# Optimization experiments

Hardware: AMD Instinct MI355X
Metric: run time of the kernel (lower is better)

The kernel has to match this reference:

```python
import jax, jax.numpy as jnp
import numpy as np

D_G, D_2D, D_3D = 512, 768, 1024
D_F, RANK, ATTN_H = 256, 16, 512
B = 8192


def _xavier(key, shape):
    fan_out, fan_in = shape
    lim = float(np.sqrt(6.0 / (fan_in + fan_out)))
    return jax.random.uniform(key, shape, jnp.float32, -lim, lim)


def setup_inputs() -> dict:
    key = jax.random.key(0)
    ks = jax.random.split(key, 12)
    inp = {
        "h_g": jax.random.normal(ks[0], (B, D_G), jnp.float32),
        "h_2d": jax.random.normal(ks[1], (B, D_2D), jnp.float32),
        "h_3d": jax.random.normal(ks[2], (B, D_3D), jnp.float32),
        # modality projections (torch Linear: y = x @ W.T + b)
        "Wg": _xavier(ks[3], (D_F, D_G)),   "bg": jnp.zeros((D_F,), jnp.float32),
        "W2": _xavier(ks[4], (D_F, D_2D)),  "b2": jnp.zeros((D_F,), jnp.float32),
        "W3": _xavier(ks[5], (D_F, D_3D)),  "b3": jnp.zeros((D_F,), jnp.float32),
        # LayerNorm affine params
        "ln_g_w": jnp.ones((D_F,), jnp.float32),  "ln_g_b": jnp.zeros((D_F,), jnp.float32),
        "ln_2_w": jnp.ones((D_F,), jnp.float32),  "ln_2_b": jnp.zeros((D_F,), jnp.float32),
        "ln_3_w": jnp.ones((D_F,), jnp.float32),  "ln_3_b": jnp.zeros((D_F,), jnp.float32),
        # rank expansions (no bias)
        "U": _xavier(ks[6], (RANK * D_F, D_F)),
        "V": _xavier(ks[7], (RANK * D_F, D_F)),
        "S": _xavier(ks[8], (RANK * D_F, D_F)),
        # attention MLP
        "Wa1": _xavier(ks[9], (ATTN_H, D_G + D_2D + D_3D)), "ba1": jnp.zeros((ATTN_H,), jnp.float32),
        "Wa2": _xavier(ks[10], (RANK, ATTN_H)),             "ba2": jnp.zeros((RANK,), jnp.float32),
    }
    return inp


def _layernorm(x, w, b, eps=1e-5):
    mu = jnp.mean(x, axis=-1, keepdims=True)
    var = jnp.var(x, axis=-1, keepdims=True)
    return (x - mu) * jax.lax.rsqrt(var + eps) * w + b


def reference(h_g, h_2d, h_3d, Wg, bg, W2, b2, W3, b3,
              ln_g_w, ln_g_b, ln_2_w, ln_2_b, ln_3_w, ln_3_b,
              U, V, S, Wa1, ba1, Wa2, ba2):
    # proj + LN + ReLU (dropout=0 / eval mode)
    g = jax.nn.relu(_layernorm(h_g @ Wg.T + bg, ln_g_w, ln_g_b))
    d2 = jax.nn.relu(_layernorm(h_2d @ W2.T + b2, ln_2_w, ln_2_b))
    d3 = jax.nn.relu(_layernorm(h_3d @ W3.T + b3, ln_3_w, ln_3_b))
    b = g.shape[0]
    # rank expansion: (B, R, d_f)
    g_r = (g @ U.T).reshape(b, RANK, D_F)
    d2_r = (d2 @ V.T).reshape(b, RANK, D_F)
    d3_r = (d3 @ S.T).reshape(b, RANK, D_F)
    z_r = g_r * d2_r * d3_r  # elementwise tri-linear product
    # rank attention from raw modality concat
    h_cat = jnp.concatenate([h_g, h_2d, h_3d], axis=-1)
    beta = jax.nn.softmax(jax.nn.relu(h_cat @ Wa1.T + ba1) @ Wa2.T + ba2, axis=-1)  # (B, R)
    z = jnp.einsum('brd,br->bd', z_r, beta)  # (B, d_f)
    return z
```

## Files before the change

### kernel.cpp

```cpp
#include <hip/hip_runtime.h>
#include <stdint.h>

#define B_ROWS 8192
#define DG 512
#define D2 768
#define D3 1024
#define DCAT 2304
#define DF 256
#define RANK 16
#define AH 512

#define OFF_WG 0
#define OFF_W2 131072
#define OFF_W3 327680
#define OFF_U  589824
#define OFF_V  1638400
#define OFF_S  2686976
#define OFF_WA1 3735552

#define WS_WBUF  0u
#define WS_HCAT  9830400u
#define WS_GBUF  9830400u
#define WS_PROJ  47579136u
#define WS_A1P   72744960u
#define WS_BETA  89522176u
#define WS_ZPART 47579136u
#define WS_REQUIRED 94240768u

typedef __attribute__((ext_vector_type(8))) short short8;
typedef __attribute__((ext_vector_type(4))) float f32x4;

__device__ inline unsigned short f2bf(float f) {
  union { float f; unsigned int u; } v; v.f = f;
  unsigned int u = v.u + 0x7fffu + ((v.u >> 16) & 1u);
  return (unsigned short)(u >> 16);
}
__device__ inline float bf2f(unsigned short h) {
  union { float f; unsigned int u; } v; v.u = ((unsigned int)h) << 16;
  return v.f;
}

typedef const unsigned int __attribute__((address_space(1)))* as1_u32p;
typedef unsigned int __attribute__((address_space(3)))* as3_u32p;

__device__ inline void g2l16(const unsigned short* g, unsigned short* l) {
  __builtin_amdgcn_global_load_lds((as1_u32p)g, (as3_u32p)l, 16, 0, 0);
}


__global__ __launch_bounds__(256) void cvt_all_k(const float* __restrict__ hg,
                                                 const float* __restrict__ h2,
                                                 const float* __restrict__ h3,
                                                 const float* __restrict__ Wg,
                                                 const float* __restrict__ W2,
                                                 const float* __restrict__ W3,
                                                 const float* __restrict__ U,
                                                 const float* __restrict__ V,
                                                 const float* __restrict__ S,
                                                 const float* __restrict__ Wa1,
                                                 unsigned short* __restrict__ hcat,
                                                 unsigned short* __restrict__ wbuf) {
  const int bid = blockIdx.x;
  if (bid < 18432) {
    const int idx = bid * 256 + threadIdx.x;
    const int e = idx * 4;
    const int row = e / DCAT;
    const int col = e - row * DCAT;
    const float* src;
    if (col < DG) src = hg + (size_t)row * DG + col;
    else if (col < DG + D2) src = h2 + (size_t)row * D2 + (col - DG);
    else src = h3 + (size_t)row * D3 + (col - DG - D2);
    float4 v = *(const float4*)src;
    ushort4 o;
    o.x = f2bf(v.x); o.y = f2bf(v.y); o.z = f2bf(v.z); o.w = f2bf(v.w);
    *(ushort4*)(hcat + e) = o;
  } else {
    const int idx = (bid - 18432) * 256 + threadIdx.x;
    const int e = idx * 4;
    const float* src;
    if (e < OFF_W2)       src = Wg  + e;
    else if (e < OFF_W3)  src = W2  + (e - OFF_W2);
    else if (e < OFF_U)   src = W3  + (e - OFF_W3);
    else if (e < OFF_V)   src = U   + (e - OFF_U);
    else if (e < OFF_S)   src = V   + (e - OFF_V);
    else if (e < OFF_WA1) src = S   + (e - OFF_S);
    else                  src = Wa1 + (e - OFF_WA1);
    float4 v = *(const float4*)src;
    ushort4 o;
    o.x = f2bf(v.x); o.y = f2bf(v.y); o.z = f2bf(v.z); o.w = f2bf(v.w);
    *(ushort4*)(wbuf + e) = o;
  }
}


__device__ __forceinline__ void gemm_mainloop(const unsigned short* Ag, int lda,
                                              const unsigned short* Bg, int ldb,
                                              int K,
                                              unsigned short* lA, unsigned short* lB,
                                              f32x4 acc[4][4]) {
  const int tid = threadIdx.x;
  const int lane = tid & 63;
  const int wr = tid >> 7;
  const int wc = (tid >> 6) & 1;
#pragma unroll
  for (int i = 0; i < 4; ++i)
#pragma unroll
    for (int j = 0; j < 4; ++j)
      acc[i][j] = (f32x4){0.f, 0.f, 0.f, 0.f};

  const int row_s = tid >> 3;
  const int kc_s = (((tid & 7) ^ ((tid >> 3) & 7)) << 3);
  const int mbase = wr * 64 + (lane & 15);
  const int nbase = wc * 64 + (lane & 15);
  const int kq = lane >> 4;
  const int h = lane & 7;

  const int nsteps = K >> 6;
  for (int ks = 0; ks < nsteps; ++ks) {
    const int k0 = ks << 6;
    __syncthreads();
#pragma unroll
    for (int p = 0; p < 4; ++p) {
      const int row = p * 32 + row_s;
      const int lofs = (p * 256 + tid) * 8;
      g2l16(Ag + (size_t)row * lda + k0 + kc_s, lA + lofs);
      g2l16(Bg + (size_t)row * ldb + k0 + kc_s, lB + lofs);
    }
    __syncthreads();
#pragma unroll
    for (int kk = 0; kk < 2; ++kk) {
      const int kch = (kk << 2) + kq;
      const int ko = ((kch ^ h) << 3);
      short8 af[4], bfr[4];
#pragma unroll
      for (int t = 0; t < 4; ++t) {
        af[t]  = *(const short8*)(lA + (mbase + t * 16) * 64 + ko);
        bfr[t] = *(const short8*)(lB + (nbase + t * 16) * 64 + ko);
      }
#pragma unroll
      for (int ti = 0; ti < 4; ++ti)
#pragma unroll
        for (int tj = 0; tj < 4; ++tj)
          acc[ti][tj] = __builtin_amdgcn_mfma_f32_16x16x32_bf16(af[ti], bfr[tj], acc[ti][tj], 0, 0, 0);
    }
  }
}


__device__ __forceinline__ void gemm_mainloop_bk128(const unsigned short* Ag, int lda,
                                                    const unsigned short* Bg, int ldb,
                                                    int K,
                                                    unsigned short* lA, unsigned short* lB,
                                                    f32x4 acc[4][4]) {
  const int tid = threadIdx.x;
  const int lane = tid & 63;
  const int wr = tid >> 7;
  const int wc = (tid >> 6) & 1;
#pragma unroll
  for (int i = 0; i < 4; ++i)
#pragma unroll
    for (int j = 0; j < 4; ++j)
      acc[i][j] = (f32x4){0.f, 0.f, 0.f, 0.f};

  const int row_s = tid >> 4;
  const int kc_s = (((tid & 15) ^ ((tid >> 4) & 15)) << 3);
  const int mbase = wr * 64 + (lane & 15);
  const int nbase = wc * 64 + (lane & 15);
  const int kq = lane >> 4;
  const int h = lane & 15;

  const int nsteps = K >> 7;
  for (int ks = 0; ks < nsteps; ++ks) {
    const int k0 = ks << 7;
    __syncthreads();
#pragma unroll
    for (int p = 0; p < 8; ++p) {
      const int row = p * 16 + row_s;
      const int lofs = (p * 256 + tid) * 8;
      g2l16(Ag + (size_t)row * lda + k0 + kc_s, lA + lofs);
      g2l16(Bg + (size_t)row * ldb + k0 + kc_s, lB + lofs);
    }
    __syncthreads();
#pragma unroll
    for (int kk = 0; kk < 4; ++kk) {
      const int kch = (kk << 2) + kq;
      const int ko = ((kch ^ h) << 3);
      short8 af[4], bfr[4];
#pragma unroll
      for (int t = 0; t < 4; ++t) {
        af[t]  = *(const short8*)(lA + (mbase + t * 16) * 128 + ko);
        bfr[t] = *(const short8*)(lB + (nbase + t * 16) * 128 + ko);
      }
#pragma unroll
      for (int ti = 0; ti < 4; ++ti)
#pragma unroll
        for (int tj = 0; tj < 4; ++tj)
          acc[ti][tj] = __builtin_amdgcn_mfma_f32_16x16x32_bf16(af[ti], bfr[tj], acc[ti][tj], 0, 0, 0);
    }
  }
}


__global__ __launch_bounds__(256) void fatgemm_k(const unsigned short* __restrict__ hcat,
                                                 const unsigned short* __restrict__ wbuf,
                                                 float* __restrict__ proj,
                                                 unsigned short* __restrict__ a1part) {
  __shared__ __align__(16) unsigned short lA[128 * 64];
  __shared__ __align__(16) unsigned short lB[128 * 64];
  const int bid = blockIdx.x;
  f32x4 acc[4][4];
  const int lane = threadIdx.x & 63;
  const int wr = threadIdx.x >> 7, wc = (threadIdx.x >> 6) & 1;

  if (bid < 384) {
    const int z = bid >> 7;
    const int local = bid & 127;
    const int m0 = (local >> 1) << 7;
    const int n0 = (local & 1) << 7;
    const int Kz   = (z == 0) ? DG : (z == 1 ? D2 : D3);
    const int aoff = (z == 0) ? 0  : (z == 1 ? DG : DG + D2);
    const int woff = (z == 0) ? OFF_WG : (z == 1 ? OFF_W2 : OFF_W3);
    gemm_mainloop(hcat + (size_t)m0 * DCAT + aoff, DCAT,
                  wbuf + woff + (size_t)n0 * Kz, Kz, Kz, lA, lB, acc);
    float* out = proj + (size_t)z * B_ROWS * DF;
    const int r0 = m0 + wr * 64 + ((lane >> 4) << 2);
    const int c0 = n0 + wc * 64 + (lane & 15);
#pragma unroll
    for (int ti = 0; ti < 4; ++ti)
#pragma unroll
      for (int tj = 0; tj < 4; ++tj)
#pragma unroll
        for (int i = 0; i < 4; ++i)
          out[(size_t)(r0 + ti * 16 + i) * DF + (c0 + tj * 16)] = acc[ti][tj][i];
  } else {
    const int t = bid - 384;
    const int half = t >> 8;
    const int local = t & 255;
    const int m0 = (local >> 2) << 7;
    const int n0 = (local & 3) << 7;
    const int koff = half * 1152;
    gemm_mainloop(hcat + (size_t)m0 * DCAT + koff, DCAT,
                  wbuf + OFF_WA1 + (size_t)n0 * DCAT + koff, DCAT, 1152, lA, lB, acc);
    unsigned short* out = a1part + (size_t)half * (B_ROWS * AH);
    const int r0 = m0 + wr * 64 + ((lane >> 4) << 2);
    const int c0 = n0 + wc * 64 + (lane & 15);
#pragma unroll
    for (int ti = 0; ti < 4; ++ti)
#pragma unroll
      for (int tj = 0; tj < 4; ++tj)
#pragma unroll
        for (int i = 0; i < 4; ++i)
          out[(size_t)(r0 + ti * 16 + i) * AH + (c0 + tj * 16)] = f2bf(acc[ti][tj][i]);
  }
}


__global__ __launch_bounds__(256) void rank_fused_k(const unsigned short* __restrict__ gbuf,
                                                    const unsigned short* __restrict__ wbuf,
                                                    const float* __restrict__ beta,
                                                    float* __restrict__ zpart) {
  __shared__ __align__(16) unsigned short lA[128 * 128];
  __shared__ __align__(16) unsigned short lB[128 * 128];
  __shared__ float lbeta[4 * 128];
  const int m0 = blockIdx.x * 128;
  const int d0 = blockIdx.y * 128;
  const int rg = blockIdx.z * 4;

  for (int i = threadIdx.x; i < 512; i += 256) {
    const int rr = i >> 7, row = i & 127;
    lbeta[i] = beta[(size_t)(m0 + row) * RANK + rg + rr];
  }

  const int lane = threadIdx.x & 63;
  const int wr = threadIdx.x >> 7, wc = (threadIdx.x >> 6) & 1;
  const int lr0 = wr * 64 + ((lane >> 4) << 2);

  f32x4 zacc[4][4];
#pragma unroll
  for (int ti = 0; ti < 4; ++ti)
#pragma unroll
    for (int tj = 0; tj < 4; ++tj)
      zacc[ti][tj] = (f32x4){0.f, 0.f, 0.f, 0.f};

  for (int rr = 0; rr < 4; ++rr) {
    const int n0 = (rg + rr) * 256 + d0;
    f32x4 prod[4][4];
    f32x4 acc[4][4];
#pragma unroll
    for (int zi = 0; zi < 3; ++zi) {
      gemm_mainloop_bk128(gbuf + (size_t)zi * B_ROWS * DF + (size_t)m0 * DF, DF,
                          wbuf + OFF_U + (size_t)zi * 1048576 + (size_t)n0 * DF, DF, DF,
                          lA, lB, acc);
      if (zi == 0) {
#pragma unroll
        for (int ti = 0; ti < 4; ++ti)
#pragma unroll
          for (int tj = 0; tj < 4; ++tj)
            prod[ti][tj] = acc[ti][tj];
      } else {
#pragma unroll
        for (int ti = 0; ti < 4; ++ti)
#pragma unroll
          for (int tj = 0; tj < 4; ++tj)
            prod[ti][tj] *= acc[ti][tj];
      }
    }
#pragma unroll
    for (int ti = 0; ti < 4; ++ti) {
      const float4 b4 = *(const float4*)(lbeta + rr * 128 + lr0 + ti * 16);
      const float bv[4] = {b4.x, b4.y, b4.z, b4.w};
#pragma unroll
      for (int tj = 0; tj < 4; ++tj)
#pragma unroll
        for (int i = 0; i < 4; ++i)
          zacc[ti][tj][i] += prod[ti][tj][i] * bv[i];
    }
  }

  float* zp = zpart + (size_t)blockIdx.z * (B_ROWS * DF);
  const int c0 = d0 + wc * 64 + (lane & 15);
#pragma unroll
  for (int ti = 0; ti < 4; ++ti)
#pragma unroll
    for (int tj = 0; tj < 4; ++tj)
#pragma unroll
      for (int i = 0; i < 4; ++i)
        zp[(size_t)(m0 + lr0 + ti * 16 + i) * DF + (c0 + tj * 16)] = zacc[ti][tj][i];
}


__global__ __launch_bounds__(256) void zsum_k(const float* __restrict__ zpart,
                                              float* __restrict__ z) {
  const int idx = blockIdx.x * 256 + threadIdx.x;
  const size_t e = (size_t)idx * 4;
  const size_t stride = (size_t)B_ROWS * DF;
  float4 a = *(const float4*)(zpart + e);
  float4 b = *(const float4*)(zpart + stride + e);
  float4 c = *(const float4*)(zpart + 2 * stride + e);
  float4 d = *(const float4*)(zpart + 3 * stride + e);
  float4 o;
  o.x = (a.x + b.x) + (c.x + d.x);
  o.y = (a.y + b.y) + (c.y + d.y);
  o.z = (a.z + b.z) + (c.z + d.z);
  o.w = (a.w + b.w) + (c.w + d.w);
  *(float4*)(z + e) = o;
}


__global__ __launch_bounds__(256) void ln_relu_k(const float* __restrict__ proj,
                                                 const float* __restrict__ bg, const float* __restrict__ b2, const float* __restrict__ b3,
                                                 const float* __restrict__ wg, const float* __restrict__ wbg,
                                                 const float* __restrict__ w2, const float* __restrict__ wb2,
                                                 const float* __restrict__ w3, const float* __restrict__ wb3,
                                                 unsigned short* __restrict__ gout) {
  const int gid = blockIdx.x * 4 + (threadIdx.x >> 6);
  const int lane = threadIdx.x & 63;
  const int z = gid >> 13;
  const int row = gid & (B_ROWS - 1);
  const float* bias = z == 0 ? bg : (z == 1 ? b2 : b3);
  const float* lw = z == 0 ? wg : (z == 1 ? w2 : w3);
  const float* lb = z == 0 ? wbg : (z == 1 ? wb2 : wb3);
  const float* x = proj + (size_t)z * B_ROWS * DF + (size_t)row * DF + lane * 4;
  float4 v = *(const float4*)x;
  float4 bb = *(const float4*)(bias + lane * 4);
  v.x += bb.x; v.y += bb.y; v.z += bb.z; v.w += bb.w;
  float s = v.x + v.y + v.z + v.w;
  float q = v.x * v.x + v.y * v.y + v.z * v.z + v.w * v.w;
#pragma unroll
  for (int m = 1; m < 64; m <<= 1) { s += __shfl_xor(s, m, 64); q += __shfl_xor(q, m, 64); }
  const float mean = s * (1.f / DF);
  const float var = q * (1.f / DF) - mean * mean;
  const float rs = rsqrtf(var + 1e-5f);
  float4 w4 = *(const float4*)(lw + lane * 4);
  float4 b4 = *(const float4*)(lb + lane * 4);
  ushort4 o;
  o.x = f2bf(fmaxf((v.x - mean) * rs * w4.x + b4.x, 0.f));
  o.y = f2bf(fmaxf((v.y - mean) * rs * w4.y + b4.y, 0.f));
  o.z = f2bf(fmaxf((v.z - mean) * rs * w4.z + b4.z, 0.f));
  o.w = f2bf(fmaxf((v.w - mean) * rs * w4.w + b4.w, 0.f));
  *(ushort4*)(gout + (size_t)z * B_ROWS * DF + (size_t)row * DF + lane * 4) = o;
}


__global__ __launch_bounds__(256) void attn_beta_k(const unsigned short* __restrict__ a1part,
                                                   const float* __restrict__ ba1,
                                                   const float* __restrict__ Wa2,
                                                   const float* __restrict__ ba2,
                                                   float* __restrict__ beta) {
  __shared__ float lw[RANK * AH];
  for (int i = threadIdx.x; i < RANK * AH / 4; i += 256)
    *(float4*)(lw + i * 4) = *(const float4*)(Wa2 + i * 4);
  __syncthreads();
  const int row = blockIdx.x * 4 + (threadIdx.x >> 6);
  const int lane = threadIdx.x & 63;
  const unsigned short* h0 = a1part + (size_t)row * AH + lane * 8;
  const unsigned short* h1 = h0 + (size_t)B_ROWS * AH;
  const uint4 p0 = *(const uint4*)h0;
  const uint4 p1 = *(const uint4*)h1;
  const unsigned int u0[4] = {p0.x, p0.y, p0.z, p0.w};
  const unsigned int u1[4] = {p1.x, p1.y, p1.z, p1.w};
  float4 ca = *(const float4*)(ba1 + lane * 8);
  float4 cb = *(const float4*)(ba1 + lane * 8 + 4);
  const float bias[8] = {ca.x, ca.y, ca.z, ca.w, cb.x, cb.y, cb.z, cb.w};
  float av[8];
#pragma unroll
  for (int j = 0; j < 4; ++j) {
    const float s0 = bf2f((unsigned short)(u0[j] & 0xffffu)) + bf2f((unsigned short)(u1[j] & 0xffffu));
    const float s1 = bf2f((unsigned short)(u0[j] >> 16)) + bf2f((unsigned short)(u1[j] >> 16));
    av[2 * j]     = fmaxf(s0 + bias[2 * j], 0.f);
    av[2 * j + 1] = fmaxf(s1 + bias[2 * j + 1], 0.f);
  }
  float lg[RANK];
#pragma unroll
  for (int r = 0; r < RANK; ++r) {
    const float* wrow = lw + r * AH + lane * 8;
    float4 wa = *(const float4*)wrow;
    float4 wb = *(const float4*)(wrow + 4);
    float p = av[0] * wa.x + av[1] * wa.y + av[2] * wa.z + av[3] * wa.w
            + av[4] * wb.x + av[5] * wb.y + av[6] * wb.z + av[7] * wb.w;
#pragma unroll
    for (int m = 1; m < 64; m <<= 1) p += __shfl_xor(p, m, 64);
    lg[r] = p + ba2[r];
  }
  float mx = lg[0];
#pragma unroll
  for (int r = 1; r < RANK; ++r) mx = fmaxf(mx, lg[r]);
  float den = 0.f;
#pragma unroll
  for (int r = 0; r < RANK; ++r) { lg[r] = __expf(lg[r] - mx); den += lg[r]; }
  const float inv = 1.f / den;
  if (lane < RANK) {
    float mine = 0.f;
#pragma unroll
    for (int r = 0; r < RANK; ++r) mine = (lane == r) ? lg[r] : mine;
    beta[(size_t)row * RANK + lane] = mine * inv;
  }
}


extern "C" void kernel_launch(void* const* d_in, const int* in_sizes, int n_in,
                              void* d_out, int out_size, void* d_ws, size_t ws_size,
                              hipStream_t stream) {
  if (ws_size < (size_t)WS_REQUIRED) return;

  const float* h_g   = (const float*)d_in[0];
  const float* h_2d  = (const float*)d_in[1];
  const float* h_3d  = (const float*)d_in[2];
  const float* Wg    = (const float*)d_in[3];
  const float* bg    = (const float*)d_in[4];
  const float* W2    = (const float*)d_in[5];
  const float* b2    = (const float*)d_in[6];
  const float* W3    = (const float*)d_in[7];
  const float* b3    = (const float*)d_in[8];
  const float* ln_g_w = (const float*)d_in[9];
  const float* ln_g_b = (const float*)d_in[10];
  const float* ln_2_w = (const float*)d_in[11];
  const float* ln_2_b = (const float*)d_in[12];
  const float* ln_3_w = (const float*)d_in[13];
  const float* ln_3_b = (const float*)d_in[14];
  const float* U     = (const float*)d_in[15];
  const float* V     = (const float*)d_in[16];
  const float* S     = (const float*)d_in[17];
  const float* Wa1   = (const float*)d_in[18];
  const float* ba1   = (const float*)d_in[19];
  const float* Wa2   = (const float*)d_in[20];
  const float* ba2   = (const float*)d_in[21];

  char* ws = (char*)d_ws;
  unsigned short* wbuf   = (unsigned short*)(ws + WS_WBUF);
  unsigned short* hcat   = (unsigned short*)(ws + WS_HCAT);
  unsigned short* gbuf   = (unsigned short*)(ws + WS_GBUF);
  float*          proj   = (float*)(ws + WS_PROJ);
  unsigned short* a1part = (unsigned short*)(ws + WS_A1P);
  float*          beta   = (float*)(ws + WS_BETA);
  float*          zpart  = (float*)(ws + WS_ZPART);
  float* z = (float*)d_out;

  cvt_all_k<<<dim3(23232), dim3(256), 0, stream>>>(h_g, h_2d, h_3d,
                                                   Wg, W2, W3, U, V, S, Wa1, hcat, wbuf);
  fatgemm_k<<<dim3(896), dim3(256), 0, stream>>>(hcat, wbuf, proj, a1part);
  ln_relu_k<<<dim3(6144), dim3(256), 0, stream>>>(proj, bg, b2, b3, ln_g_w, ln_g_b,
                                                  ln_2_w, ln_2_b, ln_3_w, ln_3_b, gbuf);
  attn_beta_k<<<dim3(2048), dim3(256), 0, stream>>>(a1part, ba1, Wa2, ba2, beta);
  rank_fused_k<<<dim3(64, 2, 4), dim3(256), 0, stream>>>(gbuf, wbuf, beta, zpart);
  zsum_k<<<dim3(2048), dim3(256), 0, stream>>>(zpart, z);
}
```

Measured before the change: 324.6 us.

## Double-buffer rank GEMM LDS stages and merge LN and attention-beta kernels

The rank-fused kernel now runs a single flattened loop over all 48 K-steps (4 ranks × 3 modalities × 4 K-chunks of 64). It double-buffers the LDS tiles so the next global-to-LDS load is issued before the current tile's MFMAs, and it needs one barrier per step instead of two. The LayerNorm/ReLU kernel and the attention softmax kernel are merged into one launch, with blocks split by index. LDS use drops from 64KB to 64KB total across two buffers of half-K, and the merged kernel carries the larger shared-memory footprint for all blocks.

```diff
diff --git a/kernel.cpp b/kernel.cpp
--- a/kernel.cpp
+++ b/kernel.cpp
@@ -147,60 +147,6 @@
 }
 
 
-__device__ __forceinline__ void gemm_mainloop_bk128(const unsigned short* Ag, int lda,
-                                                    const unsigned short* Bg, int ldb,
-                                                    int K,
-                                                    unsigned short* lA, unsigned short* lB,
-                                                    f32x4 acc[4][4]) {
-  const int tid = threadIdx.x;
-  const int lane = tid & 63;
-  const int wr = tid >> 7;
-  const int wc = (tid >> 6) & 1;
-#pragma unroll
-  for (int i = 0; i < 4; ++i)
-#pragma unroll
-    for (int j = 0; j < 4; ++j)
-      acc[i][j] = (f32x4){0.f, 0.f, 0.f, 0.f};
-
-  const int row_s = tid >> 4;
-  const int kc_s = (((tid & 15) ^ ((tid >> 4) & 15)) << 3);
-  const int mbase = wr * 64 + (lane & 15);
-  const int nbase = wc * 64 + (lane & 15);
-  const int kq = lane >> 4;
-  const int h = lane & 15;
-
-  const int nsteps = K >> 7;
-  for (int ks = 0; ks < nsteps; ++ks) {
-    const int k0 = ks << 7;
-    __syncthreads();
-#pragma unroll
-    for (int p = 0; p < 8; ++p) {
-      const int row = p * 16 + row_s;
-      const int lofs = (p * 256 + tid) * 8;
-      g2l16(Ag + (size_t)row * lda + k0 + kc_s, lA + lofs);
-      g2l16(Bg + (size_t)row * ldb + k0 + kc_s, lB + lofs);
-    }
-    __syncthreads();
-#pragma unroll
-    for (int kk = 0; kk < 4; ++kk) {
-      const int kch = (kk << 2) + kq;
-      const int ko = ((kch ^ h) << 3);
-      short8 af[4], bfr[4];
-#pragma unroll
-      for (int t = 0; t < 4; ++t) {
-        af[t]  = *(const short8*)(lA + (mbase + t * 16) * 128 + ko);
-        bfr[t] = *(const short8*)(lB + (nbase + t * 16) * 128 + ko);
-      }
-#pragma unroll
-      for (int ti = 0; ti < 4; ++ti)
-#pragma unroll
-        for (int tj = 0; tj < 4; ++tj)
-          acc[ti][tj] = __builtin_amdgcn_mfma_f32_16x16x32_bf16(af[ti], bfr[tj], acc[ti][tj], 0, 0, 0);
-    }
-  }
-}
-
-
 __global__ __launch_bounds__(256) void fatgemm_k(const unsigned short* __restrict__ hcat,
                                                  const unsigned short* __restrict__ wbuf,
                                                  float* __restrict__ proj,
@@ -259,61 +205,112 @@
                                                     const unsigned short* __restrict__ wbuf,
                                                     const float* __restrict__ beta,
                                                     float* __restrict__ zpart) {
-  __shared__ __align__(16) unsigned short lA[128 * 128];
-  __shared__ __align__(16) unsigned short lB[128 * 128];
+  __shared__ __align__(16) unsigned short lA[2 * 128 * 64];
+  __shared__ __align__(16) unsigned short lB[2 * 128 * 64];
   __shared__ float lbeta[4 * 128];
   const int m0 = blockIdx.x * 128;
   const int d0 = blockIdx.y * 128;
   const int rg = blockIdx.z * 4;
-
-  for (int i = threadIdx.x; i < 512; i += 256) {
+  const int tid = threadIdx.x;
+
+  for (int i = tid; i < 512; i += 256) {
     const int rr = i >> 7, row = i & 127;
     lbeta[i] = beta[(size_t)(m0 + row) * RANK + rg + rr];
   }
 
-  const int lane = threadIdx.x & 63;
-  const int wr = threadIdx.x >> 7, wc = (threadIdx.x >> 6) & 1;
+  const int lane = tid & 63;
+  const int wr = tid >> 7, wc = (tid >> 6) & 1;
+  const int row_s = tid >> 3;
+  const int kc_s = (((tid & 7) ^ ((tid >> 3) & 7)) << 3);
+  const int mbase = wr * 64 + (lane & 15);
+  const int nbase = wc * 64 + (lane & 15);
+  const int kq = lane >> 4;
+  const int h = lane & 7;
   const int lr0 = wr * 64 + ((lane >> 4) << 2);
 
-  f32x4 zacc[4][4];
+  auto stage = [&](int s, int buf) {
+    const int rr = s / 12;
+    const int t  = s - rr * 12;
+    const int zi = t >> 2;
+    const int ks = t & 3;
+    const unsigned short* Ag = gbuf + (size_t)zi * (B_ROWS * DF) + (size_t)m0 * DF + (ks << 6);
+    const unsigned short* Bg = wbuf + OFF_U + (size_t)zi * 1048576
+                             + (size_t)((rg + rr) * 256 + d0) * DF + (ks << 6);
+    unsigned short* dA = lA + buf * 8192;
+    unsigned short* dB = lB + buf * 8192;
+#pragma unroll
+    for (int p = 0; p < 4; ++p) {
+      const int row = p * 32 + row_s;
+      const int lofs = (p * 256 + tid) * 8;
+      g2l16(Ag + (size_t)row * DF + kc_s, dA + lofs);
+      g2l16(Bg + (size_t)row * DF + kc_s, dB + lofs);
+    }
+  };
+
+  f32x4 zacc[4][4], prod[4][4], acc[4][4];
 #pragma unroll
   for (int ti = 0; ti < 4; ++ti)
 #pragma unroll
-    for (int tj = 0; tj < 4; ++tj)
+    for (int tj = 0; tj < 4; ++tj) {
       zacc[ti][tj] = (f32x4){0.f, 0.f, 0.f, 0.f};
-
-  for (int rr = 0; rr < 4; ++rr) {
-    const int n0 = (rg + rr) * 256 + d0;
-    f32x4 prod[4][4];
-    f32x4 acc[4][4];
-#pragma unroll
-    for (int zi = 0; zi < 3; ++zi) {
-      gemm_mainloop_bk128(gbuf + (size_t)zi * B_ROWS * DF + (size_t)m0 * DF, DF,
-                          wbuf + OFF_U + (size_t)zi * 1048576 + (size_t)n0 * DF, DF, DF,
-                          lA, lB, acc);
+      acc[ti][tj]  = (f32x4){0.f, 0.f, 0.f, 0.f};
+    }
+
+  stage(0, 0);
+  for (int s = 0; s < 48; ++s) {
+    const int cur = s & 1;
+    __syncthreads();
+    if (s + 1 < 48) stage(s + 1, cur ^ 1);
+    const unsigned short* sA = lA + cur * 8192;
+    const unsigned short* sB = lB + cur * 8192;
+#pragma unroll
+    for (int kk = 0; kk < 2; ++kk) {
+      const int kch = (kk << 2) + kq;
+      const int ko = ((kch ^ h) << 3);
+      short8 af[4], bfr[4];
+#pragma unroll
+      for (int t = 0; t < 4; ++t) {
+        af[t]  = *(const short8*)(sA + (mbase + t * 16) * 64 + ko);
+        bfr[t] = *(const short8*)(sB + (nbase + t * 16) * 64 + ko);
+      }
+#pragma unroll
+      for (int ti = 0; ti < 4; ++ti)
+#pragma unroll
+        for (int tj = 0; tj < 4; ++tj)
+          acc[ti][tj] = __builtin_amdgcn_mfma_f32_16x16x32_bf16(af[ti], bfr[tj], acc[ti][tj], 0, 0, 0);
+    }
+    if ((s & 3) == 3) {
+      const int rr = s / 12;
+      const int zi = (s - rr * 12) >> 2;
       if (zi == 0) {
 #pragma unroll
         for (int ti = 0; ti < 4; ++ti)
 #pragma unroll
           for (int tj = 0; tj < 4; ++tj)
             prod[ti][tj] = acc[ti][tj];
-      } else {
+      } else if (zi == 1) {
 #pragma unroll
         for (int ti = 0; ti < 4; ++ti)
 #pragma unroll
           for (int tj = 0; tj < 4; ++tj)
             prod[ti][tj] *= acc[ti][tj];
+      } else {
+#pragma unroll
+        for (int ti = 0; ti < 4; ++ti) {
+          const float4 b4 = *(const float4*)(lbeta + rr * 128 + lr0 + ti * 16);
+          const float bv[4] = {b4.x, b4.y, b4.z, b4.w};
+#pragma unroll
+          for (int tj = 0; tj < 4; ++tj)
+#pragma unroll
+            for (int i = 0; i < 4; ++i)
+              zacc[ti][tj][i] += prod[ti][tj][i] * acc[ti][tj][i] * bv[i];
+        }
       }
-    }
-#pragma unroll
-    for (int ti = 0; ti < 4; ++ti) {
-      const float4 b4 = *(const float4*)(lbeta + rr * 128 + lr0 + ti * 16);
-      const float bv[4] = {b4.x, b4.y, b4.z, b4.w};
-#pragma unroll
-      for (int tj = 0; tj < 4; ++tj)
-#pragma unroll
-        for (int i = 0; i < 4; ++i)
-          zacc[ti][tj][i] += prod[ti][tj][i] * bv[i];
+#pragma unroll
+      for (int ti = 0; ti < 4; ++ti)
+#pragma unroll
+        for (int tj = 0; tj < 4; ++tj)
+          acc[ti][tj] = (f32x4){0.f, 0.f, 0.f, 0.f};
     }
   }
 
@@ -347,93 +344,94 @@
 }
 
 
-__global__ __launch_bounds__(256) void ln_relu_k(const float* __restrict__ proj,
-                                                 const float* __restrict__ bg, const float* __restrict__ b2, const float* __restrict__ b3,
-                                                 const float* __restrict__ wg, const float* __restrict__ wbg,
-                                                 const float* __restrict__ w2, const float* __restrict__ wb2,
-                                                 const float* __restrict__ w3, const float* __restrict__ wb3,
-                                                 unsigned short* __restrict__ gout) {
-  const int gid = blockIdx.x * 4 + (threadIdx.x >> 6);
-  const int lane = threadIdx.x & 63;
-  const int z = gid >> 13;
-  const int row = gid & (B_ROWS - 1);
-  const float* bias = z == 0 ? bg : (z == 1 ? b2 : b3);
-  const float* lw = z == 0 ? wg : (z == 1 ? w2 : w3);
-  const float* lb = z == 0 ? wbg : (z == 1 ? wb2 : wb3);
-  const float* x = proj + (size_t)z * B_ROWS * DF + (size_t)row * DF + lane * 4;
-  float4 v = *(const float4*)x;
-  float4 bb = *(const float4*)(bias + lane * 4);
-  v.x += bb.x; v.y += bb.y; v.z += bb.z; v.w += bb.w;
-  float s = v.x + v.y + v.z + v.w;
-  float q = v.x * v.x + v.y * v.y + v.z * v.z + v.w * v.w;
-#pragma unroll
-  for (int m = 1; m < 64; m <<= 1) { s += __shfl_xor(s, m, 64); q += __shfl_xor(q, m, 64); }
-  const float mean = s * (1.f / DF);
-  const float var = q * (1.f / DF) - mean * mean;
-  const float rs = rsqrtf(var + 1e-5f);
-  float4 w4 = *(const float4*)(lw + lane * 4);
-  float4 b4 = *(const float4*)(lb + lane * 4);
-  ushort4 o;
-  o.x = f2bf(fmaxf((v.x - mean) * rs * w4.x + b4.x, 0.f));
-  o.y = f2bf(fmaxf((v.y - mean) * rs * w4.y + b4.y, 0.f));
-  o.z = f2bf(fmaxf((v.z - mean) * rs * w4.z + b4.z, 0.f));
-  o.w = f2bf(fmaxf((v.w - mean) * rs * w4.w + b4.w, 0.f));
-  *(ushort4*)(gout + (size_t)z * B_ROWS * DF + (size_t)row * DF + lane * 4) = o;
-}
-
-
-__global__ __launch_bounds__(256) void attn_beta_k(const unsigned short* __restrict__ a1part,
-                                                   const float* __restrict__ ba1,
-                                                   const float* __restrict__ Wa2,
-                                                   const float* __restrict__ ba2,
-                                                   float* __restrict__ beta) {
-  __shared__ float lw[RANK * AH];
-  for (int i = threadIdx.x; i < RANK * AH / 4; i += 256)
-    *(float4*)(lw + i * 4) = *(const float4*)(Wa2 + i * 4);
-  __syncthreads();
-  const int row = blockIdx.x * 4 + (threadIdx.x >> 6);
-  const int lane = threadIdx.x & 63;
-  const unsigned short* h0 = a1part + (size_t)row * AH + lane * 8;
-  const unsigned short* h1 = h0 + (size_t)B_ROWS * AH;
-  const uint4 p0 = *(const uint4*)h0;
-  const uint4 p1 = *(const uint4*)h1;
-  const unsigned int u0[4] = {p0.x, p0.y, p0.z, p0.w};
-  const unsigned int u1[4] = {p1.x, p1.y, p1.z, p1.w};
-  float4 ca = *(const float4*)(ba1 + lane * 8);
-  float4 cb = *(const float4*)(ba1 + lane * 8 + 4);
-  const float bias[8] = {ca.x, ca.y, ca.z, ca.w, cb.x, cb.y, cb.z, cb.w};
-  float av[8];
-#pragma unroll
-  for (int j = 0; j < 4; ++j) {
-    const float s0 = bf2f((unsigned short)(u0[j] & 0xffffu)) + bf2f((unsigned short)(u1[j] & 0xffffu));
-    const float s1 = bf2f((unsigned short)(u0[j] >> 16)) + bf2f((unsigned short)(u1[j] >> 16));
-    av[2 * j]     = fmaxf(s0 + bias[2 * j], 0.f);
-    av[2 * j + 1] = fmaxf(s1 + bias[2 * j + 1], 0.f);
-  }
-  float lg[RANK];
-#pragma unroll
-  for (int r = 0; r < RANK; ++r) {
-    const float* wrow = lw + r * AH + lane * 8;
-    float4 wa = *(const float4*)wrow;
-    float4 wb = *(const float4*)(wrow + 4);
-    float p = av[0] * wa.x + av[1] * wa.y + av[2] * wa.z + av[3] * wa.w
-            + av[4] * wb.x + av[5] * wb.y + av[6] * wb.z + av[7] * wb.w;
-#pragma unroll
-    for (int m = 1; m < 64; m <<= 1) p += __shfl_xor(p, m, 64);
-    lg[r] = p + ba2[r];
-  }
-  float mx = lg[0];
-#pragma unroll
-  for (int r = 1; r < RANK; ++r) mx = fmaxf(mx, lg[r]);
-  float den = 0.f;
-#pragma unroll
-  for (int r = 0; r < RANK; ++r) { lg[r] = __expf(lg[r] - mx); den += lg[r]; }
-  const float inv = 1.f / den;
-  if (lane < RANK) {
-    float mine = 0.f;
-#pragma unroll
-    for (int r = 0; r < RANK; ++r) mine = (lane == r) ? lg[r] : mine;
-    beta[(size_t)row * RANK + lane] = mine * inv;
+__global__ __launch_bounds__(256) void post_k(const float* __restrict__ proj,
+                                              const float* __restrict__ bg, const float* __restrict__ b2, const float* __restrict__ b3,
+                                              const float* __restrict__ wg, const float* __restrict__ wbg,
+                                              const float* __restrict__ w2, const float* __restrict__ wb2,
+                                              const float* __restrict__ w3, const float* __restrict__ wb3,
+                                              unsigned short* __restrict__ gout,
+                                              const unsigned short* __restrict__ a1part,
+                                              const float* __restrict__ ba1,
+                                              const float* __restrict__ Wa2,
+                                              const float* __restrict__ ba2,
+                                              float* __restrict__ beta) {
+  const int bid = blockIdx.x;
+  if (bid < 6144) {
+    const int gid = bid * 4 + (threadIdx.x >> 6);
+    const int lane = threadIdx.x & 63;
+    const int z = gid >> 13;
+    const int row = gid & (B_ROWS - 1);
+    const float* bias = z == 0 ? bg : (z == 1 ? b2 : b3);
+    const float* lw = z == 0 ? wg : (z == 1 ? w2 : w3);
+    const float* lb = z == 0 ? wbg : (z == 1 ? wb2 : wb3);
+    const float* x = proj + (size_t)z * B_ROWS * DF + (size_t)row * DF + lane * 4;
+    float4 v = *(const float4*)x;
+    float4 bb = *(const float4*)(bias + lane * 4);
+    v.x += bb.x; v.y += bb.y; v.z += bb.z; v.w += bb.w;
+    float s = v.x + v.y + v.z + v.w;
+    float q = v.x * v.x + v.y * v.y + v.z * v.z + v.w * v.w;
+#pragma unroll
+    for (int m = 1; m < 64; m <<= 1) { s += __shfl_xor(s, m, 64); q += __shfl_xor(q, m, 64); }
+    const float mean = s * (1.f / DF);
+    const float var = q * (1.f / DF) - mean * mean;
+    const float rs = rsqrtf(var + 1e-5f);
+    float4 w4 = *(const float4*)(lw + lane * 4);
+    float4 b4 = *(const float4*)(lb + lane * 4);
+    ushort4 o;
+    o.x = f2bf(fmaxf((v.x - mean) * rs * w4.x + b4.x, 0.f));
+    o.y = f2bf(fmaxf((v.y - mean) * rs * w4.y + b4.y, 0.f));
+    o.z = f2bf(fmaxf((v.z - mean) * rs * w4.z + b4.z, 0.f));
+    o.w = f2bf(fmaxf((v.w - mean) * rs * w4.w + b4.w, 0.f));
+    *(ushort4*)(gout + (size_t)z * B_ROWS * DF + (size_t)row * DF + lane * 4) = o;
+  } else {
+    __shared__ float lw[RANK * AH];
+    for (int i = threadIdx.x; i < RANK * AH / 4; i += 256)
+      *(float4*)(lw + i * 4) = *(const float4*)(Wa2 + i * 4);
+    __syncthreads();
+    const int row = (bid - 6144) * 4 + (threadIdx.x >> 6);
+    const int lane = threadIdx.x & 63;
+    const unsigned short* h0 = a1part + (size_t)row * AH + lane * 8;
+    const unsigned short* h1 = h0 + (size_t)B_ROWS * AH;
+    const uint4 p0 = *(const uint4*)h0;
+    const uint4 p1 = *(const uint4*)h1;
+    const unsigned int u0[4] = {p0.x, p0.y, p0.z, p0.w};
+    const unsigned int u1[4] = {p1.x, p1.y, p1.z, p1.w};
+    float4 ca = *(const float4*)(ba1 + lane * 8);
+    float4 cb = *(const float4*)(ba1 + lane * 8 + 4);
+    const float bias[8] = {ca.x, ca.y, ca.z, ca.w, cb.x, cb.y, cb.z, cb.w};
+    float av[8];
+#pragma unroll
+    for (int j = 0; j < 4; ++j) {
+      const float s0 = bf2f((unsigned short)(u0[j] & 0xffffu)) + bf2f((unsigned short)(u1[j] & 0xffffu));
+      const float s1 = bf2f((unsigned short)(u0[j] >> 16)) + bf2f((unsigned short)(u1[j] >> 16));
+      av[2 * j]     = fmaxf(s0 + bias[2 * j], 0.f);
+      av[2 * j + 1] = fmaxf(s1 + bias[2 * j + 1], 0.f);
+    }
+    float lg[RANK];
+#pragma unroll
+    for (int r = 0; r < RANK; ++r) {
+      const float* wrow = lw + r * AH + lane * 8;
+      float4 wa = *(const float4*)wrow;
+      float4 wb = *(const float4*)(wrow + 4);
+      float p = av[0] * wa.x + av[1] * wa.y + av[2] * wa.z + av[3] * wa.w
+              + av[4] * wb.x + av[5] * wb.y + av[6] * wb.z + av[7] * wb.w;
+#pragma unroll
+      for (int m = 1; m < 64; m <<= 1) p += __shfl_xor(p, m, 64);
+      lg[r] = p + ba2[r];
+    }
+    float mx = lg[0];
+#pragma unroll
+    for (int r = 1; r < RANK; ++r) mx = fmaxf(mx, lg[r]);
+    float den = 0.f;
+#pragma unroll
+    for (int r = 0; r < RANK; ++r) { lg[r] = __expf(lg[r] - mx); den += lg[r]; }
+    const float inv = 1.f / den;
+    if (lane < RANK) {
+      float mine = 0.f;
+#pragma unroll
+      for (int r = 0; r < RANK; ++r) mine = (lane == r) ? lg[r] : mine;
+      beta[(size_t)row * RANK + lane] = mine * inv;
+    }
   }
 }
 
@@ -479,9 +477,9 @@
   cvt_all_k<<<dim3(23232), dim3(256), 0, stream>>>(h_g, h_2d, h_3d,
                                                    Wg, W2, W3, U, V, S, Wa1, hcat, wbuf);
   fatgemm_k<<<dim3(896), dim3(256), 0, stream>>>(hcat, wbuf, proj, a1part);
-  ln_relu_k<<<dim3(6144), dim3(256), 0, stream>>>(proj, bg, b2, b3, ln_g_w, ln_g_b,
-                                                  ln_2_w, ln_2_b, ln_3_w, ln_3_b, gbuf);
-  attn_beta_k<<<dim3(2048), dim3(256), 0, stream>>>(a1part, ba1, Wa2, ba2, beta);
+  post_k<<<dim3(8192), dim3(256), 0, stream>>>(proj, bg, b2, b3, ln_g_w, ln_g_b,
+                                               ln_2_w, ln_2_b, ln_3_w, ln_3_b, gbuf,
+                                               a1part, ba1, Wa2, ba2, beta);
   rank_fused_k<<<dim3(64, 2, 4), dim3(256), 0, stream>>>(gbuf, wbuf, beta, zpart);
   zsum_k<<<dim3(2048), dim3(256), 0, stream>>>(zpart, z);
 }
```

Result: slower. 348.5 us (+7.4%).

## Store modality inputs as separate bf16 buffers and merge LN and attention kernels

Applied to the files above, without the earlier changes.

The conversion kernel now writes each modality input into its own contiguous bf16 buffer instead of one interleaved concat matrix, which removes the per-element row/column divide and branch. The projection GEMM reads these directly with a natural stride. The attention GEMM runs two back-to-back accumulating mainloops over the g and 2d parts for one half and the 3d part for the other. The LayerNorm/ReLU and attention-softmax kernels are merged into one launch to save a kernel launch and let the two overlap. The risk is that the merged kernel's attention blocks reserve LDS that the LN blocks do not need, which can lower occupancy, and that the split mainloops add extra sync points.

```diff
diff --git a/kernel.cpp b/kernel.cpp
--- a/kernel.cpp
+++ b/kernel.cpp
@@ -19,7 +19,9 @@
 #define OFF_WA1 3735552
 
 #define WS_WBUF  0u
-#define WS_HCAT  9830400u
+#define WS_HG    9830400u
+#define WS_H2    18219008u
+#define WS_H3    30801920u
 #define WS_GBUF  9830400u
 #define WS_PROJ  47579136u
 #define WS_A1P   72744960u
@@ -48,36 +50,32 @@
 }
 
 
-__global__ __launch_bounds__(256) void cvt_all_k(const float* __restrict__ hg,
-                                                 const float* __restrict__ h2,
-                                                 const float* __restrict__ h3,
-                                                 const float* __restrict__ Wg,
-                                                 const float* __restrict__ W2,
-                                                 const float* __restrict__ W3,
-                                                 const float* __restrict__ U,
-                                                 const float* __restrict__ V,
-                                                 const float* __restrict__ S,
-                                                 const float* __restrict__ Wa1,
-                                                 unsigned short* __restrict__ hcat,
-                                                 unsigned short* __restrict__ wbuf) {
+__global__ __launch_bounds__(256) void cvt_split_k(const float* __restrict__ hg,
+                                                   const float* __restrict__ h2,
+                                                   const float* __restrict__ h3,
+                                                   const float* __restrict__ Wg,
+                                                   const float* __restrict__ W2,
+                                                   const float* __restrict__ W3,
+                                                   const float* __restrict__ U,
+                                                   const float* __restrict__ V,
+                                                   const float* __restrict__ S,
+                                                   const float* __restrict__ Wa1,
+                                                   unsigned short* __restrict__ hgb,
+                                                   unsigned short* __restrict__ h2b,
+                                                   unsigned short* __restrict__ h3b,
+                                                   unsigned short* __restrict__ wbuf) {
   const int bid = blockIdx.x;
+  const float* src;
+  unsigned short* dst;
+  int e;
   if (bid < 18432) {
-    const int idx = bid * 256 + threadIdx.x;
-    const int e = idx * 4;
-    const int row = e / DCAT;
-    const int col = e - row * DCAT;
-    const float* src;
-    if (col < DG) src = hg + (size_t)row * DG + col;
-    else if (col < DG + D2) src = h2 + (size_t)row * D2 + (col - DG);
-    else src = h3 + (size_t)row * D3 + (col - DG - D2);
-    float4 v = *(const float4*)src;
-    ushort4 o;
-    o.x = f2bf(v.x); o.y = f2bf(v.y); o.z = f2bf(v.z); o.w = f2bf(v.w);
-    *(ushort4*)(hcat + e) = o;
+    e = (bid * 256 + threadIdx.x) * 4;
+    if (e < 4194304)        { src = hg + e;            dst = hgb + e; }
+    else if (e < 10485760)  { src = h2 + (e - 4194304); dst = h2b + (e - 4194304); }
+    else                    { src = h3 + (e - 10485760); dst = h3b + (e - 10485760); }
   } else {
-    const int idx = (bid - 18432) * 256 + threadIdx.x;
-    const int e = idx * 4;
-    const float* src;
+    e = ((bid - 18432) * 256 + threadIdx.x) * 4;
+    dst = wbuf + e;
     if (e < OFF_W2)       src = Wg  + e;
     else if (e < OFF_W3)  src = W2  + (e - OFF_W2);
     else if (e < OFF_U)   src = W3  + (e - OFF_W3);
@@ -85,29 +83,23 @@
     else if (e < OFF_S)   src = V   + (e - OFF_V);
     else if (e < OFF_WA1) src = S   + (e - OFF_S);
     else                  src = Wa1 + (e - OFF_WA1);
-    float4 v = *(const float4*)src;
-    ushort4 o;
-    o.x = f2bf(v.x); o.y = f2bf(v.y); o.z = f2bf(v.z); o.w = f2bf(v.w);
-    *(ushort4*)(wbuf + e) = o;
-  }
-}
-
-
-__device__ __forceinline__ void gemm_mainloop(const unsigned short* Ag, int lda,
-                                              const unsigned short* Bg, int ldb,
-                                              int K,
-                                              unsigned short* lA, unsigned short* lB,
-                                              f32x4 acc[4][4]) {
+  }
+  float4 v = *(const float4*)src;
+  ushort4 o;
+  o.x = f2bf(v.x); o.y = f2bf(v.y); o.z = f2bf(v.z); o.w = f2bf(v.w);
+  *(ushort4*)dst = o;
+}
+
+
+__device__ __forceinline__ void gemm_mainloop_acc(const unsigned short* Ag, int lda,
+                                                  const unsigned short* Bg, int ldb,
+                                                  int K,
+                                                  unsigned short* lA, unsigned short* lB,
+                                                  f32x4 acc[4][4]) {
   const int tid = threadIdx.x;
   const int lane = tid & 63;
   const int wr = tid >> 7;
   const int wc = (tid >> 6) & 1;
-#pragma unroll
-  for (int i = 0; i < 4; ++i)
-#pragma unroll
-    for (int j = 0; j < 4; ++j)
-      acc[i][j] = (f32x4){0.f, 0.f, 0.f, 0.f};
-
   const int row_s = tid >> 3;
   const int kc_s = (((tid & 7) ^ ((tid >> 3) & 7)) << 3);
   const int mbase = wr * 64 + (lane & 15);
@@ -144,6 +136,14 @@
           acc[ti][tj] = __builtin_amdgcn_mfma_f32_16x16x32_bf16(af[ti], bfr[tj], acc[ti][tj], 0, 0, 0);
     }
   }
+}
+
+__device__ __forceinline__ void zero_acc(f32x4 acc[4][4]) {
+#pragma unroll
+  for (int i = 0; i < 4; ++i)
+#pragma unroll
+    for (int j = 0; j < 4; ++j)
+      acc[i][j] = (f32x4){0.f, 0.f, 0.f, 0.f};
 }
 
 
@@ -201,7 +201,9 @@
 }
 
 
-__global__ __launch_bounds__(256) void fatgemm_k(const unsigned short* __restrict__ hcat,
+__global__ __launch_bounds__(256) void fatgemm_k(const unsigned short* __restrict__ hgb,
+                                                 const unsigned short* __restrict__ h2b,
+                                                 const unsigned short* __restrict__ h3b,
                                                  const unsigned short* __restrict__ wbuf,
                                                  float* __restrict__ proj,
                                                  unsigned short* __restrict__ a1part) {
@@ -211,6 +213,7 @@
   f32x4 acc[4][4];
   const int lane = threadIdx.x & 63;
   const int wr = threadIdx.x >> 7, wc = (threadIdx.x >> 6) & 1;
+  zero_acc(acc);
 
   if (bid < 384) {
     const int z = bid >> 7;
@@ -218,10 +221,10 @@
     const int m0 = (local >> 1) << 7;
     const int n0 = (local & 1) << 7;
     const int Kz   = (z == 0) ? DG : (z == 1 ? D2 : D3);
-    const int aoff = (z == 0) ? 0  : (z == 1 ? DG : DG + D2);
+    const unsigned short* Ab = (z == 0) ? hgb : (z == 1 ? h2b : h3b);
     const int woff = (z == 0) ? OFF_WG : (z == 1 ? OFF_W2 : OFF_W3);
-    gemm_mainloop(hcat + (size_t)m0 * DCAT + aoff, DCAT,
-                  wbuf + woff + (size_t)n0 * Kz, Kz, Kz, lA, lB, acc);
+    gemm_mainloop_acc(Ab + (size_t)m0 * Kz, Kz,
+                      wbuf + woff + (size_t)n0 * Kz, Kz, Kz, lA, lB, acc);
     float* out = proj + (size_t)z * B_ROWS * DF;
     const int r0 = m0 + wr * 64 + ((lane >> 4) << 2);
     const int c0 = n0 + wc * 64 + (lane & 15);
@@ -238,9 +241,13 @@
     const int local = t & 255;
     const int m0 = (local >> 2) << 7;
     const int n0 = (local & 3) << 7;
-    const int koff = half * 1152;
-    gemm_mainloop(hcat + (size_t)m0 * DCAT + koff, DCAT,
-                  wbuf + OFF_WA1 + (size_t)n0 * DCAT + koff, DCAT, 1152, lA, lB, acc);
+    const unsigned short* Bb = wbuf + OFF_WA1 + (size_t)n0 * DCAT;
+    if (half == 0) {
+      gemm_mainloop_acc(hgb + (size_t)m0 * DG, DG, Bb, DCAT, DG, lA, lB, acc);
+      gemm_mainloop_acc(h2b + (size_t)m0 * D2, D2, Bb + DG, DCAT, D2, lA, lB, acc);
+    } else {
+      gemm_mainloop_acc(h3b + (size_t)m0 * D3, D3, Bb + DG + D2, DCAT, D3, lA, lB, acc);
+    }
     unsigned short* out = a1part + (size_t)half * (B_ROWS * AH);
     const int r0 = m0 + wr * 64 + ((lane >> 4) << 2);
     const int c0 = n0 + wc * 64 + (lane & 15);
@@ -347,93 +354,94 @@
 }
 
 
-__global__ __launch_bounds__(256) void ln_relu_k(const float* __restrict__ proj,
-                                                 const float* __restrict__ bg, const float* __restrict__ b2, const float* __restrict__ b3,
-                                                 const float* __restrict__ wg, const float* __restrict__ wbg,
-                                                 const float* __restrict__ w2, const float* __restrict__ wb2,
-                                                 const float* __restrict__ w3, const float* __restrict__ wb3,
-                                                 unsigned short* __restrict__ gout) {
-  const int gid = blockIdx.x * 4 + (threadIdx.x >> 6);
-  const int lane = threadIdx.x & 63;
-  const int z = gid >> 13;
-  const int row = gid & (B_ROWS - 1);
-  const float* bias = z == 0 ? bg : (z == 1 ? b2 : b3);
-  const float* lw = z == 0 ? wg : (z == 1 ? w2 : w3);
-  const float* lb = z == 0 ? wbg : (z == 1 ? wb2 : wb3);
-  const float* x = proj + (size_t)z * B_ROWS * DF + (size_t)row * DF + lane * 4;
-  float4 v = *(const float4*)x;
-  float4 bb = *(const float4*)(bias + lane * 4);
-  v.x += bb.x; v.y += bb.y; v.z += bb.z; v.w += bb.w;
-  float s = v.x + v.y + v.z + v.w;
-  float q = v.x * v.x + v.y * v.y + v.z * v.z + v.w * v.w;
-#pragma unroll
-  for (int m = 1; m < 64; m <<= 1) { s += __shfl_xor(s, m, 64); q += __shfl_xor(q, m, 64); }
-  const float mean = s * (1.f / DF);
-  const float var = q * (1.f / DF) - mean * mean;
-  const float rs = rsqrtf(var + 1e-5f);
-  float4 w4 = *(const float4*)(lw + lane * 4);
-  float4 b4 = *(const float4*)(lb + lane * 4);
-  ushort4 o;
-  o.x = f2bf(fmaxf((v.x - mean) * rs * w4.x + b4.x, 0.f));
-  o.y = f2bf(fmaxf((v.y - mean) * rs * w4.y + b4.y, 0.f));
-  o.z = f2bf(fmaxf((v.z - mean) * rs * w4.z + b4.z, 0.f));
-  o.w = f2bf(fmaxf((v.w - mean) * rs * w4.w + b4.w, 0.f));
-  *(ushort4*)(gout + (size_t)z * B_ROWS * DF + (size_t)row * DF + lane * 4) = o;
-}
-
-
-__global__ __launch_bounds__(256) void attn_beta_k(const unsigned short* __restrict__ a1part,
-                                                   const float* __restrict__ ba1,
-                                                   const float* __restrict__ Wa2,
-                                                   const float* __restrict__ ba2,
-                                                   float* __restrict__ beta) {
-  __shared__ float lw[RANK * AH];
-  for (int i = threadIdx.x; i < RANK * AH / 4; i += 256)
-    *(float4*)(lw + i * 4) = *(const float4*)(Wa2 + i * 4);
-  __syncthreads();
-  const int row = blockIdx.x * 4 + (threadIdx.x >> 6);
-  const int lane = threadIdx.x & 63;
-  const unsigned short* h0 = a1part + (size_t)row * AH + lane * 8;
-  const unsigned short* h1 = h0 + (size_t)B_ROWS * AH;
-  const uint4 p0 = *(const uint4*)h0;
-  const uint4 p1 = *(const uint4*)h1;
-  const unsigned int u0[4] = {p0.x, p0.y, p0.z, p0.w};
-  const unsigned int u1[4] = {p1.x, p1.y, p1.z, p1.w};
-  float4 ca = *(const float4*)(ba1 + lane * 8);
-  float4 cb = *(const float4*)(ba1 + lane * 8 + 4);
-  const float bias[8] = {ca.x, ca.y, ca.z, ca.w, cb.x, cb.y, cb.z, cb.w};
-  float av[8];
-#pragma unroll
-  for (int j = 0; j < 4; ++j) {
-    const float s0 = bf2f((unsigned short)(u0[j] & 0xffffu)) + bf2f((unsigned short)(u1[j] & 0xffffu));
-    const float s1 = bf2f((unsigned short)(u0[j] >> 16)) + bf2f((unsigned short)(u1[j] >> 16));
-    av[2 * j]     = fmaxf(s0 + bias[2 * j], 0.f);
-    av[2 * j + 1] = fmaxf(s1 + bias[2 * j + 1], 0.f);
-  }
-  float lg[RANK];
-#pragma unroll
-  for (int r = 0; r < RANK; ++r) {
-    const float* wrow = lw + r * AH + lane * 8;
-    float4 wa = *(const float4*)wrow;
-    float4 wb = *(const float4*)(wrow + 4);
-    float p = av[0] * wa.x + av[1] * wa.y + av[2] * wa.z + av[3] * wa.w
-            + av[4] * wb.x + av[5] * wb.y + av[6] * wb.z + av[7] * wb.w;
-#pragma unroll
-    for (int m = 1; m < 64; m <<= 1) p += __shfl_xor(p, m, 64);
-    lg[r] = p + ba2[r];
-  }
-  float mx = lg[0];
-#pragma unroll
-  for (int r = 1; r < RANK; ++r) mx = fmaxf(mx, lg[r]);
-  float den = 0.f;
-#pragma unroll
-  for (int r = 0; r < RANK; ++r) { lg[r] = __expf(lg[r] - mx); den += lg[r]; }
-  const float inv = 1.f / den;
-  if (lane < RANK) {
-    float mine = 0.f;
-#pragma unroll
-    for (int r = 0; r < RANK; ++r) mine = (lane == r) ? lg[r] : mine;
-    beta[(size_t)row * RANK + lane] = mine * inv;
+__global__ __launch_bounds__(256) void post_k(const float* __restrict__ proj,
+                                              const float* __restrict__ bg, const float* __restrict__ b2, const float* __restrict__ b3,
+                                              const float* __restrict__ wg, const float* __restrict__ wbg,
+                                              const float* __restrict__ w2, const float* __restrict__ wb2,
+                                              const float* __restrict__ w3, const float* __restrict__ wb3,
+                                              unsigned short* __restrict__ gout,
+                                              const unsigned short* __restrict__ a1part,
+                                              const float* __restrict__ ba1,
+                                              const float* __restrict__ Wa2,
+                                              const float* __restrict__ ba2,
+                                              float* __restrict__ beta) {
+  const int bid = blockIdx.x;
+  if (bid < 6144) {
+    const int gid = bid * 4 + (threadIdx.x >> 6);
+    const int lane = threadIdx.x & 63;
+    const int z = gid >> 13;
+    const int row = gid & (B_ROWS - 1);
+    const float* bias = z == 0 ? bg : (z == 1 ? b2 : b3);
+    const float* lw = z == 0 ? wg : (z == 1 ? w2 : w3);
+    const float* lb = z == 0 ? wbg : (z == 1 ? wb2 : wb3);
+    const float* x = proj + (size_t)z * B_ROWS * DF + (size_t)row * DF + lane * 4;
+    float4 v = *(const float4*)x;
+    float4 bb = *(const float4*)(bias + lane * 4);
+    v.x += bb.x; v.y += bb.y; v.z += bb.z; v.w += bb.w;
+    float s = v.x + v.y + v.z + v.w;
+    float q = v.x * v.x + v.y * v.y + v.z * v.z + v.w * v.w;
+#pragma unroll
+    for (int m = 1; m < 64; m <<= 1) { s += __shfl_xor(s, m, 64); q += __shfl_xor(q, m, 64); }
+    const float mean = s * (1.f / DF);
+    const float var = q * (1.f / DF) - mean * mean;
+    const float rs = rsqrtf(var + 1e-5f);
+    float4 w4 = *(const float4*)(lw + lane * 4);
+    float4 b4 = *(const float4*)(lb + lane * 4);
+    ushort4 o;
+    o.x = f2bf(fmaxf((v.x - mean) * rs * w4.x + b4.x, 0.f));
+    o.y = f2bf(fmaxf((v.y - mean) * rs * w4.y + b4.y, 0.f));
+    o.z = f2bf(fmaxf((v.z - mean) * rs * w4.z + b4.z, 0.f));
+    o.w = f2bf(fmaxf((v.w - mean) * rs * w4.w + b4.w, 0.f));
+    *(ushort4*)(gout + (size_t)z * B_ROWS * DF + (size_t)row * DF + lane * 4) = o;
+  } else {
+    __shared__ float lw[RANK * AH];
+    for (int i = threadIdx.x; i < RANK * AH / 4; i += 256)
+      *(float4*)(lw + i * 4) = *(const float4*)(Wa2 + i * 4);
+    __syncthreads();
+    const int row = (bid - 6144) * 4 + (threadIdx.x >> 6);
+    const int lane = threadIdx.x & 63;
+    const unsigned short* h0 = a1part + (size_t)row * AH + lane * 8;
+    const unsigned short* h1 = h0 + (size_t)B_ROWS * AH;
+    const uint4 p0 = *(const uint4*)h0;
+    const uint4 p1 = *(const uint4*)h1;
+    const unsigned int u0[4] = {p0.x, p0.y, p0.z, p0.w};
+    const unsigned int u1[4] = {p1.x, p1.y, p1.z, p1.w};
+    float4 ca = *(const float4*)(ba1 + lane * 8);
+    float4 cb = *(const float4*)(ba1 + lane * 8 + 4);
+    const float bias[8] = {ca.x, ca.y, ca.z, ca.w, cb.x, cb.y, cb.z, cb.w};
+    float av[8];
+#pragma unroll
+    for (int j = 0; j < 4; ++j) {
+      const float s0 = bf2f((unsigned short)(u0[j] & 0xffffu)) + bf2f((unsigned short)(u1[j] & 0xffffu));
+      const float s1 = bf2f((unsigned short)(u0[j] >> 16)) + bf2f((unsigned short)(u1[j] >> 16));
+      av[2 * j]     = fmaxf(s0 + bias[2 * j], 0.f);
+      av[2 * j + 1] = fmaxf(s1 + bias[2 * j + 1], 0.f);
+    }
+    float lg[RANK];
+#pragma unroll
+    for (int r = 0; r < RANK; ++r) {
+      const float* wrow = lw + r * AH + lane * 8;
+      float4 wa = *(const float4*)wrow;
+      float4 wb = *(const float4*)(wrow + 4);
+      float p = av[0] * wa.x + av[1] * wa.y + av[2] * wa.z + av[3] * wa.w
+              + av[4] * wb.x + av[5] * wb.y + av[6] * wb.z + av[7] * wb.w;
+#pragma unroll
+      for (int m = 1; m < 64; m <<= 1) p += __shfl_xor(p, m, 64);
+      lg[r] = p + ba2[r];
+    }
+    float mx = lg[0];
+#pragma unroll
+    for (int r = 1; r < RANK; ++r) mx = fmaxf(mx, lg[r]);
+    float den = 0.f;
+#pragma unroll
+    for (int r = 0; r < RANK; ++r) { lg[r] = __expf(lg[r] - mx); den += lg[r]; }
+    const float inv = 1.f / den;
+    if (lane < RANK) {
+      float mine = 0.f;
+#pragma unroll
+      for (int r = 0; r < RANK; ++r) mine = (lane == r) ? lg[r] : mine;
+      beta[(size_t)row * RANK + lane] = mine * inv;
+    }
   }
 }
 
@@ -468,7 +476,9 @@
 
   char* ws = (char*)d_ws;
   unsigned short* wbuf   = (unsigned short*)(ws + WS_WBUF);
-  unsigned short* hcat   = (unsigned short*)(ws + WS_HCAT);
+  unsigned short* hgb    = (unsigned short*)(ws + WS_HG);
+  unsigned short* h2b    = (unsigned short*)(ws + WS_H2);
+  unsigned short* h3b    = (unsigned short*)(ws + WS_H3);
   unsigned short* gbuf   = (unsigned short*)(ws + WS_GBUF);
   float*          proj   = (float*)(ws + WS_PROJ);
   unsigned short* a1part = (unsigned short*)(ws + WS_A1P);
@@ -476,12 +486,13 @@
   float*          zpart  = (float*)(ws + WS_ZPART);
   float* z = (float*)d_out;
 
-  cvt_all_k<<<dim3(23232), dim3(256), 0, stream>>>(h_g, h_2d, h_3d,
-                                                   Wg, W2, W3, U, V, S, Wa1, hcat, wbuf);
-  fatgemm_k<<<dim3(896), dim3(256), 0, stream>>>(hcat, wbuf, proj, a1part);
-  ln_relu_k<<<dim3(6144), dim3(256), 0, stream>>>(proj, bg, b2, b3, ln_g_w, ln_g_b,
-                                                  ln_2_w, ln_2_b, ln_3_w, ln_3_b, gbuf);
-  attn_beta_k<<<dim3(2048), dim3(256), 0, stream>>>(a1part, ba1, Wa2, ba2, beta);
+  cvt_split_k<<<dim3(23232), dim3(256), 0, stream>>>(h_g, h_2d, h_3d,
+                                                     Wg, W2, W3, U, V, S, Wa1,
+                                                     hgb, h2b, h3b, wbuf);
+  fatgemm_k<<<dim3(896), dim3(256), 0, stream>>>(hgb, h2b, h3b, wbuf, proj, a1part);
+  post_k<<<dim3(8192), dim3(256), 0, stream>>>(proj, bg, b2, b3, ln_g_w, ln_g_b,
+                                               ln_2_w, ln_2_b, ln_3_w, ln_3_b, gbuf,
+                                               a1part, ba1, Wa2, ba2, beta);
   rank_fused_k<<<dim3(64, 2, 4), dim3(256), 0, stream>>>(gbuf, wbuf, beta, zpart);
   zsum_k<<<dim3(2048), dim3(256), 0, stream>>>(zpart, z);
 }
```

Result: no change. 322.9 us (-0.5%).
